# Kernel optimization log

Hardware: AMD Instinct MI355X
Metric: run time of the kernel (lower is better)

## Reference

```python
import jax, jax.numpy as jnp
import numpy as np

N_NODES = 50000
N_EDGES = 600000
DIM = 128
NUM_CLASSES = 10
EPS = 1e-15
MAX_NORM = 1.0 - 1e-5  # keep points strictly inside the unit ball for artanh


def _norm(x):
    return jnp.maximum(jnp.linalg.norm(x, axis=-1, keepdims=True), EPS)


def logmap0(x):
    # Poincare ball, c=1: artanh(||x||) * x / ||x||
    n = _norm(x)
    return jnp.arctanh(jnp.minimum(n, MAX_NORM)) * x / n


def expmap0(u):
    # Poincare ball, c=1: tanh(||u||) * u / ||u||
    n = _norm(u)
    return jnp.tanh(n) * u / n


def hyp_conv(x, W, b, src, dst):
    t = logmap0(x)                       # [N, D] manifold -> tangent at origin
    h = t @ W.T + b                      # [N, D] linear in tangent space
    y = expmap0(h)                       # [N, D] back to manifold
    # message passing: gather source features, scatter-add at destinations
    return jax.ops.segment_sum(y[src], dst, num_segments=N_NODES)


def setup_inputs() -> dict:
    key = jax.random.key(0)
    ks = jax.random.split(key, 8)
    edge_index = jax.random.randint(ks[0], (2, N_EDGES), 0, N_NODES, dtype=jnp.int64)
    # entity embeddings: small tangent vectors mapped onto the ball
    x = expmap0(0.01 * jax.random.normal(ks[1], (N_NODES, DIM), dtype=jnp.float32))
    s = 1.0 / np.sqrt(DIM)
    W1 = jax.random.normal(ks[2], (DIM, DIM), dtype=jnp.float32) * s
    b1 = jax.random.normal(ks[3], (DIM,), dtype=jnp.float32) * 0.01
    W2 = jax.random.normal(ks[4], (DIM, DIM), dtype=jnp.float32) * s
    b2 = jax.random.normal(ks[5], (DIM,), dtype=jnp.float32) * 0.01
    Wc = jax.random.normal(ks[6], (NUM_CLASSES, DIM), dtype=jnp.float32) * s
    bc = jax.random.normal(ks[7], (NUM_CLASSES,), dtype=jnp.float32) * 0.01
    return {"edge_index": edge_index, "x": x, "W1": W1, "b1": b1,
            "W2": W2, "b2": b2, "Wc": Wc, "bc": bc}


def reference(edge_index, x, W1, b1, W2, b2, Wc, bc):
    src, dst = edge_index[0], edge_index[1]
    h = hyp_conv(x, W1, b1, src, dst)
    h = jax.nn.relu(h)
    h = hyp_conv(h, W2, b2, src, dst)
    h = jax.nn.relu(h)
    t = logmap0(h)
    return t @ Wc.T + bc  # [N_NODES, NUM_CLASSES]
```

## Files before the change

### kernel.cpp

```cpp
#include <hip/hip_runtime.h>

#define N_NODES 50000
#define N_EDGES 600000
#define DIM 128
#define NCLS 10
#define ELLW 64
#define CURSTRIDE 16
#define EPSF 1e-15f
#define MAXNORM 0.99999f
#define NTILE ((N_NODES + 63) / 64)
#define FILLB 586
#define XFB 512

typedef __attribute__((ext_vector_type(8))) short bf16x8;
typedef __attribute__((ext_vector_type(4))) float f32x4;

__device__ inline float waveSum(float v) {
#pragma unroll
  for (int o = 1; o < 64; o <<= 1) v += __shfl_xor(v, o, 64);
  return v;
}

__device__ inline unsigned short f2bf(float f) {
  union { float f; unsigned u; } c; c.f = f;
  return (unsigned short)((c.u + 0x7FFFu + ((c.u >> 16) & 1u)) >> 16);
}
__device__ inline float bf_lo(unsigned u) {
  union { unsigned u; float f; } c; c.u = u << 16; return c.f;
}
__device__ inline float bf_hi(unsigned u) {
  union { unsigned u; float f; } c; c.u = u & 0xFFFF0000u; return c.f;
}

__global__ __launch_bounds__(256) void init_kernel(
    int* __restrict__ cursor, const float* __restrict__ W1, const float* __restrict__ W2,
    unsigned short* __restrict__ W1b, unsigned short* __restrict__ W2b)
{
  int i = blockIdx.x * 256 + threadIdx.x;
  if (i < N_NODES) cursor[i * CURSTRIDE] = 0;
  if (i < DIM * DIM) {
    W1b[i] = f2bf(W1[i]);
    W2b[i] = f2bf(W2[i]);
  }
}

__global__ __launch_bounds__(256, 2) void fill_transform(
    const int* __restrict__ src, const int* __restrict__ dst,
    int* __restrict__ cursor, unsigned short* __restrict__ ell,
    const float* __restrict__ x, const unsigned short* __restrict__ Wb,
    const float* __restrict__ b, unsigned short* __restrict__ y)
{
  __shared__ __align__(16) unsigned short At[64 * DIM];

  if (blockIdx.x < FILLB) {
    const int nthr = FILLB * 256;
    const int e = blockIdx.x * 256 + threadIdx.x;
    const int e0 = e, e1 = e + nthr, e2 = e + 2 * nthr, e3 = e + 3 * nthr;
    int d0, d1, d2, d3, s0, s1, s2, s3;
    if (e0 < N_EDGES) { d0 = dst[e0]; s0 = src[e0]; }
    if (e1 < N_EDGES) { d1 = dst[e1]; s1 = src[e1]; }
    if (e2 < N_EDGES) { d2 = dst[e2]; s2 = src[e2]; }
    if (e3 < N_EDGES) { d3 = dst[e3]; s3 = src[e3]; }
    int p0, p1, p2, p3;
    if (e0 < N_EDGES) p0 = atomicAdd(&cursor[d0 * CURSTRIDE], 1);
    if (e1 < N_EDGES) p1 = atomicAdd(&cursor[d1 * CURSTRIDE], 1);
    if (e2 < N_EDGES) p2 = atomicAdd(&cursor[d2 * CURSTRIDE], 1);
    if (e3 < N_EDGES) p3 = atomicAdd(&cursor[d3 * CURSTRIDE], 1);
    if (e0 < N_EDGES) ell[(size_t)d0 * ELLW + p0] = (unsigned short)s0;
    if (e1 < N_EDGES) ell[(size_t)d1 * ELLW + p1] = (unsigned short)s1;
    if (e2 < N_EDGES) ell[(size_t)d2 * ELLW + p2] = (unsigned short)s2;
    if (e3 < N_EDGES) ell[(size_t)d3 * ELLW + p3] = (unsigned short)s3;
    return;
  }

  const int tid = threadIdx.x;
  const int w = tid >> 6;
  const int l = tid & 63;
  const int lr = l & 15;
  const int lg = l >> 4;

  bf16x8 bf[8][4];
#pragma unroll
  for (int n = 0; n < 8; ++n)
#pragma unroll
    for (int kc = 0; kc < 4; ++kc)
      bf[n][kc] = *(const bf16x8*)(Wb + (n * 16 + lr) * DIM + kc * 32 + lg * 8);

  float bias[8];
#pragma unroll
  for (int n = 0; n < 8; ++n) bias[n] = b[n * 16 + lr];

  const int row = w * 16 + lr;

  for (int tile = blockIdx.x - FILLB; tile < NTILE; tile += XFB) {
    const int base = tile * 64;
    const int node = base + row;
    __syncthreads();

    float v[32];
    if (node < N_NODES) {
      const float4* xr = (const float4*)(x + (size_t)node * DIM + lg * 32);
#pragma unroll
      for (int q = 0; q < 8; ++q) {
        float4 f = xr[q];
        v[q * 4 + 0] = f.x; v[q * 4 + 1] = f.y; v[q * 4 + 2] = f.z; v[q * 4 + 3] = f.w;
      }
    } else {
#pragma unroll
      for (int q = 0; q < 32; ++q) v[q] = 0.f;
    }
    float sq = 0.f;
#pragma unroll
    for (int q = 0; q < 32; ++q) sq += v[q] * v[q];
    sq += __shfl_xor(sq, 16, 64);
    sq += __shfl_xor(sq, 32, 64);
    float n1 = sqrtf(sq);
    float nc = fmaxf(n1, EPSF);
    float nm = fminf(nc, MAXNORM);
    float scale = 0.5f * logf((1.f + nm) / (1.f - nm)) / nc;
#pragma unroll
    for (int s = 0; s < 4; ++s) {
      unsigned short tmp[8];
#pragma unroll
      for (int e = 0; e < 8; ++e) tmp[e] = f2bf(v[s * 8 + e] * scale);
      int byte = row * 256 + lg * 64 + s * 16;
      byte ^= (row & 7) << 4;
      *(bf16x8*)((char*)At + byte) = *(const bf16x8*)tmp;
    }
    __syncthreads();

    f32x4 acc[8];
#pragma unroll
    for (int n = 0; n < 8; ++n) {
      acc[n][0] = bias[n]; acc[n][1] = bias[n]; acc[n][2] = bias[n]; acc[n][3] = bias[n];
    }
#pragma unroll
    for (int kc = 0; kc < 4; ++kc) {
      int byte = row * 256 + kc * 64 + lg * 16;
      byte ^= (row & 7) << 4;
      bf16x8 af = *(const bf16x8*)((const char*)At + byte);
#pragma unroll
      for (int n = 0; n < 8; ++n)
        acc[n] = __builtin_amdgcn_mfma_f32_16x16x32_bf16(af, bf[n][kc], acc[n], 0, 0, 0);
    }

    float rs[4];
#pragma unroll
    for (int j = 0; j < 4; ++j) {
      float s2 = 0.f;
#pragma unroll
      for (int n = 0; n < 8; ++n) s2 += acc[n][j] * acc[n][j];
      s2 += __shfl_xor(s2, 1, 64);
      s2 += __shfl_xor(s2, 2, 64);
      s2 += __shfl_xor(s2, 4, 64);
      s2 += __shfl_xor(s2, 8, 64);
      float n2 = sqrtf(s2);
      float n2c = fmaxf(n2, EPSF);
      rs[j] = tanhf(n2c) / n2c;
    }
#pragma unroll
    for (int j = 0; j < 4; ++j) {
      int nrow = base + w * 16 + lg * 4 + j;
      if (nrow < N_NODES) {
        unsigned short* yr = y + (size_t)nrow * DIM + lr;
#pragma unroll
        for (int n = 0; n < 8; ++n) yr[n * 16] = f2bf(acc[n][j] * rs[j]);
      }
    }
  }
}

__global__ __launch_bounds__(256) void gatherT_kernel(
    const unsigned short* __restrict__ y, const int* __restrict__ cursor,
    const unsigned short* __restrict__ ell, unsigned short* __restrict__ tout)
{
  const int wave = threadIdx.x >> 6;
  const int lane = threadIdx.x & 63;
  const int nodeA = blockIdx.x * 8 + wave * 2;
  const int nodeB = nodeA + 1;

  const int cntA = cursor[nodeA * CURSTRIDE];
  const int cntB = cursor[nodeB * CURSTRIDE];
  const int idxA = (int)ell[(size_t)nodeA * ELLW + lane];
  const int idxB = (int)ell[(size_t)nodeB * ELLW + lane];

  float2 aA0 = {0.f, 0.f}, aA1 = {0.f, 0.f};
  float2 aB0 = {0.f, 0.f}, aB1 = {0.f, 0.f};

  unsigned uA[16], uB[16];
#pragma unroll
  for (int q = 0; q < 16; ++q) {
    int sA = __shfl(idxA, q, 64);
    int sB = __shfl(idxB, q, 64);
    uA[q] = ((const unsigned*)(y + (size_t)sA * DIM))[lane];
    uB[q] = ((const unsigned*)(y + (size_t)sB * DIM))[lane];
  }
#pragma unroll
  for (int q = 0; q < 16; ++q) {
    float vx = (q < cntA) ? bf_lo(uA[q]) : 0.f;
    float vy = (q < cntA) ? bf_hi(uA[q]) : 0.f;
    float wx = (q < cntB) ? bf_lo(uB[q]) : 0.f;
    float wy = (q < cntB) ? bf_hi(uB[q]) : 0.f;
    if (q & 1) { aA1.x += vx; aA1.y += vy; aB1.x += wx; aB1.y += wy; }
    else       { aA0.x += vx; aA0.y += vy; aB0.x += wx; aB0.y += wy; }
  }
  const int mx = max(cntA, cntB);
  for (int j = 16; j < mx; j += 8) {
    unsigned tA[8], tB[8];
#pragma unroll
    for (int q = 0; q < 8; ++q) {
      int sA = __shfl(idxA, j + q, 64);
      int sB = __shfl(idxB, j + q, 64);
      tA[q] = ((const unsigned*)(y + (size_t)sA * DIM))[lane];
      tB[q] = ((const unsigned*)(y + (size_t)sB * DIM))[lane];
    }
#pragma unroll
    for (int q = 0; q < 8; ++q) {
      if (j + q < cntA) { aA0.x += bf_lo(tA[q]); aA0.y += bf_hi(tA[q]); }
      if (j + q < cntB) { aB0.x += bf_lo(tB[q]); aB0.y += bf_hi(tB[q]); }
    }
  }

  float2 rA, rB;
  rA.x = fmaxf(aA0.x + aA1.x, 0.f);  rA.y = fmaxf(aA0.y + aA1.y, 0.f);
  rB.x = fmaxf(aB0.x + aB1.x, 0.f);  rB.y = fmaxf(aB0.y + aB1.y, 0.f);

  float sA = waveSum(rA.x * rA.x + rA.y * rA.y);
  float sB = waveSum(rB.x * rB.x + rB.y * rB.y);

  float nA = fmaxf(sqrtf(sA), EPSF);
  float nmA = fminf(nA, MAXNORM);
  float scA = 0.5f * logf((1.0f + nmA) / (1.0f - nmA)) / nA;
  float nB = fmaxf(sqrtf(sB), EPSF);
  float nmB = fminf(nB, MAXNORM);
  float scB = 0.5f * logf((1.0f + nmB) / (1.0f - nmB)) / nB;

  unsigned oA = (unsigned)f2bf(rA.x * scA) | ((unsigned)f2bf(rA.y * scA) << 16);
  unsigned oB = (unsigned)f2bf(rB.x * scB) | ((unsigned)f2bf(rB.y * scB) << 16);
  ((unsigned*)(tout + (size_t)nodeA * DIM))[lane] = oA;
  ((unsigned*)(tout + (size_t)nodeB * DIM))[lane] = oB;
}

__global__ __launch_bounds__(256, 2) void transform2_mfma(
    const unsigned short* __restrict__ t, const unsigned short* __restrict__ Wb,
    const float* __restrict__ b, unsigned short* __restrict__ y)
{
  const int tid = threadIdx.x;
  const int w = tid >> 6;
  const int l = tid & 63;
  const int lr = l & 15;
  const int lg = l >> 4;

  __shared__ __align__(16) unsigned short At[64 * DIM];

  bf16x8 bf[8][4];
#pragma unroll
  for (int n = 0; n < 8; ++n)
#pragma unroll
    for (int kc = 0; kc < 4; ++kc)
      bf[n][kc] = *(const bf16x8*)(Wb + (n * 16 + lr) * DIM + kc * 32 + lg * 8);

  float bias[8];
#pragma unroll
  for (int n = 0; n < 8; ++n) bias[n] = b[n * 16 + lr];

  const int row = w * 16 + lr;

  for (int tile = blockIdx.x; tile < NTILE; tile += gridDim.x) {
    const int base = tile * 64;
    const int node = base + row;
    __syncthreads();

#pragma unroll
    for (int s = 0; s < 4; ++s) {
      bf16x8 frag;
      if (node < N_NODES)
        frag = *(const bf16x8*)(t + (size_t)node * DIM + lg * 32 + s * 8);
      else
        frag = bf16x8{0, 0, 0, 0, 0, 0, 0, 0};
      int byte = row * 256 + lg * 64 + s * 16;
      byte ^= (row & 7) << 4;
      *(bf16x8*)((char*)At + byte) = frag;
    }
    __syncthreads();

    f32x4 acc[8];
#pragma unroll
    for (int n = 0; n < 8; ++n) {
      acc[n][0] = bias[n]; acc[n][1] = bias[n]; acc[n][2] = bias[n]; acc[n][3] = bias[n];
    }
#pragma unroll
    for (int kc = 0; kc < 4; ++kc) {
      int byte = row * 256 + kc * 64 + lg * 16;
      byte ^= (row & 7) << 4;
      bf16x8 af = *(const bf16x8*)((const char*)At + byte);
#pragma unroll
      for (int n = 0; n < 8; ++n)
        acc[n] = __builtin_amdgcn_mfma_f32_16x16x32_bf16(af, bf[n][kc], acc[n], 0, 0, 0);
    }

    float rs[4];
#pragma unroll
    for (int j = 0; j < 4; ++j) {
      float s2 = 0.f;
#pragma unroll
      for (int n = 0; n < 8; ++n) s2 += acc[n][j] * acc[n][j];
      s2 += __shfl_xor(s2, 1, 64);
      s2 += __shfl_xor(s2, 2, 64);
      s2 += __shfl_xor(s2, 4, 64);
      s2 += __shfl_xor(s2, 8, 64);
      float n2 = sqrtf(s2);
      float n2c = fmaxf(n2, EPSF);
      rs[j] = tanhf(n2c) / n2c;
    }
#pragma unroll
    for (int j = 0; j < 4; ++j) {
      int nrow = base + w * 16 + lg * 4 + j;
      if (nrow < N_NODES) {
        unsigned short* yr = y + (size_t)nrow * DIM + lr;
#pragma unroll
        for (int n = 0; n < 8; ++n) yr[n * 16] = f2bf(acc[n][j] * rs[j]);
      }
    }
  }
}

__global__ __launch_bounds__(256) void head_mfma(
    const unsigned short* __restrict__ t2, const float* __restrict__ Wc,
    const float* __restrict__ bc, float* __restrict__ out)
{
  const int base = blockIdx.x * 64;
  const int w = threadIdx.x >> 6;
  const int l = threadIdx.x & 63;
  const int lr = l & 15;
  const int lg = l >> 4;

  bf16x8 bw[4];
#pragma unroll
  for (int kc = 0; kc < 4; ++kc) {
    unsigned short tmp[8];
    if (lr < NCLS) {
      const float* wr = Wc + (size_t)lr * DIM + kc * 32 + lg * 8;
#pragma unroll
      for (int e = 0; e < 8; ++e) tmp[e] = f2bf(wr[e]);
    } else {
#pragma unroll
      for (int e = 0; e < 8; ++e) tmp[e] = 0;
    }
    bw[kc] = *(const bf16x8*)tmp;
  }
  const float bias = (lr < NCLS) ? bc[lr] : 0.f;

  const int arow = base + w * 16 + lr;
  f32x4 acc;
  acc[0] = bias; acc[1] = bias; acc[2] = bias; acc[3] = bias;
#pragma unroll
  for (int kc = 0; kc < 4; ++kc) {
    bf16x8 af;
    if (arow < N_NODES)
      af = *(const bf16x8*)(t2 + (size_t)arow * DIM + kc * 32 + lg * 8);
    else
      af = bf16x8{0, 0, 0, 0, 0, 0, 0, 0};
    acc = __builtin_amdgcn_mfma_f32_16x16x32_bf16(af, bw[kc], acc, 0, 0, 0);
  }

  if (lr < NCLS) {
#pragma unroll
    for (int j = 0; j < 4; ++j) {
      int nrow = base + w * 16 + lg * 4 + j;
      if (nrow < N_NODES) out[(size_t)nrow * NCLS + lr] = acc[j];
    }
  }
}

extern "C" void kernel_launch(void* const* d_in, const int* in_sizes, int n_in,
                              void* d_out, int out_size, void* d_ws, size_t ws_size,
                              hipStream_t stream)
{
  const int* edge = (const int*)d_in[0];
  const int* src = edge;
  const int* dst = edge + N_EDGES;
  const float* x  = (const float*)d_in[1];
  const float* W1 = (const float*)d_in[2];
  const float* b1 = (const float*)d_in[3];
  const float* W2 = (const float*)d_in[4];
  const float* b2 = (const float*)d_in[5];
  const float* Wc = (const float*)d_in[6];
  const float* bc = (const float*)d_in[7];
  float* out = (float*)d_out;

  unsigned short* ybuf = (unsigned short*)d_ws;
  unsigned short* tbuf = ybuf + (size_t)N_NODES * DIM;
  unsigned short* W1b = tbuf + (size_t)N_NODES * DIM;
  unsigned short* W2b = W1b + DIM * DIM;
  unsigned short* ell = W2b + DIM * DIM;
  int* cursor = (int*)(ell + (size_t)N_NODES * ELLW);

  init_kernel<<<(N_NODES + 255) / 256, 256, 0, stream>>>(cursor, W1, W2, W1b, W2b);

  fill_transform<<<FILLB + XFB, 256, 0, stream>>>(src, dst, cursor, ell, x, W1b, b1, ybuf);

  gatherT_kernel<<<N_NODES / 8, 256, 0, stream>>>(ybuf, cursor, ell, tbuf);

  transform2_mfma<<<512, 256, 0, stream>>>(tbuf, W2b, b2, ybuf);

  gatherT_kernel<<<N_NODES / 8, 256, 0, stream>>>(ybuf, cursor, ell, tbuf);

  head_mfma<<<NTILE, 256, 0, stream>>>(tbuf, Wc, bc, out);
}
```

Measured before the change: 127.2 us.

## Split node range to overlap gather of one half with dense transform of other

Each gather pass is split at a node boundary. The second half of the gather runs in the same launch as the dense transform (or the classifier head) of the first half, which the previous launch already gathered. A separate y2 buffer removes the in-place overwrite of ybuf so the two phases can coexist. This is meant to fill idle compute units and cut the tail of the memory-bound gather, at the cost of more launches and a mixed-role kernel that runs with the transform's launch bounds and shared memory.

```diff
diff --git a/kernel.cpp b/kernel.cpp
--- a/kernel.cpp
+++ b/kernel.cpp
@@ -8,9 +8,13 @@
 #define CURSTRIDE 16
 #define EPSF 1e-15f
 #define MAXNORM 0.99999f
-#define NTILE ((N_NODES + 63) / 64)
+#define NTILE 782
 #define FILLB 586
 #define XFB 512
+#define SPLIT 30784
+#define STILE 481
+#define GA_BLKS 3848
+#define GB_BLKS 2402
 
 typedef __attribute__((ext_vector_type(8))) short bf16x8;
 typedef __attribute__((ext_vector_type(4))) float f32x4;
@@ -170,13 +174,14 @@
   }
 }
 
-__global__ __launch_bounds__(256) void gatherT_kernel(
+__device__ __forceinline__ void do_gather2(
     const unsigned short* __restrict__ y, const int* __restrict__ cursor,
-    const unsigned short* __restrict__ ell, unsigned short* __restrict__ tout)
-{
-  const int wave = threadIdx.x >> 6;
+    const unsigned short* __restrict__ ell, unsigned short* __restrict__ tout,
+    int blkid, int nodeLo)
+{
+  const int wave = (int)threadIdx.x >> 6;
   const int lane = threadIdx.x & 63;
-  const int nodeA = blockIdx.x * 8 + wave * 2;
+  const int nodeA = nodeLo + blkid * 8 + wave * 2;
   const int nodeB = nodeA + 1;
 
   const int cntA = cursor[nodeA * CURSTRIDE];
@@ -241,17 +246,19 @@
   ((unsigned*)(tout + (size_t)nodeB * DIM))[lane] = oB;
 }
 
-__global__ __launch_bounds__(256, 2) void transform2_mfma(
+__device__ __forceinline__ void do_t2_tile(
     const unsigned short* __restrict__ t, const unsigned short* __restrict__ Wb,
-    const float* __restrict__ b, unsigned short* __restrict__ y)
+    const float* __restrict__ b, unsigned short* __restrict__ y,
+    unsigned short* At, int tile)
 {
   const int tid = threadIdx.x;
   const int w = tid >> 6;
   const int l = tid & 63;
   const int lr = l & 15;
   const int lg = l >> 4;
-
-  __shared__ __align__(16) unsigned short At[64 * DIM];
+  const int base = tile * 64;
+  const int row = w * 16 + lr;
+  const int node = base + row;
 
   bf16x8 bf[8][4];
 #pragma unroll
@@ -264,73 +271,65 @@
 #pragma unroll
   for (int n = 0; n < 8; ++n) bias[n] = b[n * 16 + lr];
 
-  const int row = w * 16 + lr;
-
-  for (int tile = blockIdx.x; tile < NTILE; tile += gridDim.x) {
-    const int base = tile * 64;
-    const int node = base + row;
-    __syncthreads();
-
-#pragma unroll
-    for (int s = 0; s < 4; ++s) {
-      bf16x8 frag;
-      if (node < N_NODES)
-        frag = *(const bf16x8*)(t + (size_t)node * DIM + lg * 32 + s * 8);
-      else
-        frag = bf16x8{0, 0, 0, 0, 0, 0, 0, 0};
-      int byte = row * 256 + lg * 64 + s * 16;
-      byte ^= (row & 7) << 4;
-      *(bf16x8*)((char*)At + byte) = frag;
-    }
-    __syncthreads();
-
-    f32x4 acc[8];
-#pragma unroll
-    for (int n = 0; n < 8; ++n) {
-      acc[n][0] = bias[n]; acc[n][1] = bias[n]; acc[n][2] = bias[n]; acc[n][3] = bias[n];
-    }
-#pragma unroll
-    for (int kc = 0; kc < 4; ++kc) {
-      int byte = row * 256 + kc * 64 + lg * 16;
-      byte ^= (row & 7) << 4;
-      bf16x8 af = *(const bf16x8*)((const char*)At + byte);
-#pragma unroll
-      for (int n = 0; n < 8; ++n)
-        acc[n] = __builtin_amdgcn_mfma_f32_16x16x32_bf16(af, bf[n][kc], acc[n], 0, 0, 0);
-    }
-
-    float rs[4];
-#pragma unroll
-    for (int j = 0; j < 4; ++j) {
-      float s2 = 0.f;
-#pragma unroll
-      for (int n = 0; n < 8; ++n) s2 += acc[n][j] * acc[n][j];
-      s2 += __shfl_xor(s2, 1, 64);
-      s2 += __shfl_xor(s2, 2, 64);
-      s2 += __shfl_xor(s2, 4, 64);
-      s2 += __shfl_xor(s2, 8, 64);
-      float n2 = sqrtf(s2);
-      float n2c = fmaxf(n2, EPSF);
-      rs[j] = tanhf(n2c) / n2c;
-    }
-#pragma unroll
-    for (int j = 0; j < 4; ++j) {
-      int nrow = base + w * 16 + lg * 4 + j;
-      if (nrow < N_NODES) {
-        unsigned short* yr = y + (size_t)nrow * DIM + lr;
-#pragma unroll
-        for (int n = 0; n < 8; ++n) yr[n * 16] = f2bf(acc[n][j] * rs[j]);
-      }
-    }
-  }
-}
-
-__global__ __launch_bounds__(256) void head_mfma(
+#pragma unroll
+  for (int s = 0; s < 4; ++s) {
+    bf16x8 frag;
+    if (node < N_NODES)
+      frag = *(const bf16x8*)(t + (size_t)node * DIM + lg * 32 + s * 8);
+    else
+      frag = bf16x8{0, 0, 0, 0, 0, 0, 0, 0};
+    int byte = row * 256 + lg * 64 + s * 16;
+    byte ^= (row & 7) << 4;
+    *(bf16x8*)((char*)At + byte) = frag;
+  }
+  __syncthreads();
+
+  f32x4 acc[8];
+#pragma unroll
+  for (int n = 0; n < 8; ++n) {
+    acc[n][0] = bias[n]; acc[n][1] = bias[n]; acc[n][2] = bias[n]; acc[n][3] = bias[n];
+  }
+#pragma unroll
+  for (int kc = 0; kc < 4; ++kc) {
+    int byte = row * 256 + kc * 64 + lg * 16;
+    byte ^= (row & 7) << 4;
+    bf16x8 af = *(const bf16x8*)((const char*)At + byte);
+#pragma unroll
+    for (int n = 0; n < 8; ++n)
+      acc[n] = __builtin_amdgcn_mfma_f32_16x16x32_bf16(af, bf[n][kc], acc[n], 0, 0, 0);
+  }
+
+  float rs[4];
+#pragma unroll
+  for (int j = 0; j < 4; ++j) {
+    float s2 = 0.f;
+#pragma unroll
+    for (int n = 0; n < 8; ++n) s2 += acc[n][j] * acc[n][j];
+    s2 += __shfl_xor(s2, 1, 64);
+    s2 += __shfl_xor(s2, 2, 64);
+    s2 += __shfl_xor(s2, 4, 64);
+    s2 += __shfl_xor(s2, 8, 64);
+    float n2 = sqrtf(s2);
+    float n2c = fmaxf(n2, EPSF);
+    rs[j] = tanhf(n2c) / n2c;
+  }
+#pragma unroll
+  for (int j = 0; j < 4; ++j) {
+    int nrow = base + w * 16 + lg * 4 + j;
+    if (nrow < N_NODES) {
+      unsigned short* yr = y + (size_t)nrow * DIM + lr;
+#pragma unroll
+      for (int n = 0; n < 8; ++n) yr[n * 16] = f2bf(acc[n][j] * rs[j]);
+    }
+  }
+}
+
+__device__ __forceinline__ void do_head_tile(
     const unsigned short* __restrict__ t2, const float* __restrict__ Wc,
-    const float* __restrict__ bc, float* __restrict__ out)
-{
-  const int base = blockIdx.x * 64;
-  const int w = threadIdx.x >> 6;
+    const float* __restrict__ bc, float* __restrict__ out, int tile)
+{
+  const int base = tile * 64;
+  const int w = (int)threadIdx.x >> 6;
   const int l = threadIdx.x & 63;
   const int lr = l & 15;
   const int lg = l >> 4;
@@ -371,6 +370,57 @@
       if (nrow < N_NODES) out[(size_t)nrow * NCLS + lr] = acc[j];
     }
   }
+}
+
+
+__global__ __launch_bounds__(256) void gather_range(
+    const unsigned short* __restrict__ y, const int* __restrict__ cursor,
+    const unsigned short* __restrict__ ell, unsigned short* __restrict__ tout,
+    int nodeLo)
+{
+  do_gather2(y, cursor, ell, tout, blockIdx.x, nodeLo);
+}
+
+__global__ __launch_bounds__(256, 2) void g1B_t2A(
+    const unsigned short* __restrict__ ybuf, const int* __restrict__ cursor,
+    const unsigned short* __restrict__ ell, unsigned short* __restrict__ tbuf,
+    const unsigned short* __restrict__ W2b, const float* __restrict__ b2,
+    unsigned short* __restrict__ y2buf)
+{
+  __shared__ __align__(16) unsigned short At[64 * DIM];
+  if (blockIdx.x < GB_BLKS) {
+    do_gather2(ybuf, cursor, ell, tbuf, blockIdx.x, SPLIT);
+  } else {
+    do_t2_tile(tbuf, W2b, b2, y2buf, At, blockIdx.x - GB_BLKS);
+  }
+}
+
+__global__ __launch_bounds__(256, 2) void t2B_kernel(
+    const unsigned short* __restrict__ tbuf, const unsigned short* __restrict__ W2b,
+    const float* __restrict__ b2, unsigned short* __restrict__ y2buf)
+{
+  __shared__ __align__(16) unsigned short At[64 * DIM];
+  do_t2_tile(tbuf, W2b, b2, y2buf, At, STILE + blockIdx.x);
+}
+
+__global__ __launch_bounds__(256) void g2B_headA(
+    const unsigned short* __restrict__ y2buf, const int* __restrict__ cursor,
+    const unsigned short* __restrict__ ell, unsigned short* __restrict__ tbuf,
+    const float* __restrict__ Wc, const float* __restrict__ bc,
+    float* __restrict__ out)
+{
+  if (blockIdx.x < GB_BLKS) {
+    do_gather2(y2buf, cursor, ell, tbuf, blockIdx.x, SPLIT);
+  } else {
+    do_head_tile(tbuf, Wc, bc, out, blockIdx.x - GB_BLKS);
+  }
+}
+
+__global__ __launch_bounds__(256) void headB_kernel(
+    const unsigned short* __restrict__ tbuf, const float* __restrict__ Wc,
+    const float* __restrict__ bc, float* __restrict__ out)
+{
+  do_head_tile(tbuf, Wc, bc, out, STILE + blockIdx.x);
 }
 
 extern "C" void kernel_launch(void* const* d_in, const int* in_sizes, int n_in,
@@ -389,9 +439,10 @@
   const float* bc = (const float*)d_in[7];
   float* out = (float*)d_out;
 
-  unsigned short* ybuf = (unsigned short*)d_ws;
-  unsigned short* tbuf = ybuf + (size_t)N_NODES * DIM;
-  unsigned short* W1b = tbuf + (size_t)N_NODES * DIM;
+  unsigned short* ybuf  = (unsigned short*)d_ws;
+  unsigned short* tbuf  = ybuf + (size_t)N_NODES * DIM;
+  unsigned short* y2buf = tbuf + (size_t)N_NODES * DIM;
+  unsigned short* W1b = y2buf + (size_t)N_NODES * DIM;
   unsigned short* W2b = W1b + DIM * DIM;
   unsigned short* ell = W2b + DIM * DIM;
   int* cursor = (int*)(ell + (size_t)N_NODES * ELLW);
@@ -400,11 +451,15 @@
 
   fill_transform<<<FILLB + XFB, 256, 0, stream>>>(src, dst, cursor, ell, x, W1b, b1, ybuf);
 
-  gatherT_kernel<<<N_NODES / 8, 256, 0, stream>>>(ybuf, cursor, ell, tbuf);
-
-  transform2_mfma<<<512, 256, 0, stream>>>(tbuf, W2b, b2, ybuf);
-
-  gatherT_kernel<<<N_NODES / 8, 256, 0, stream>>>(ybuf, cursor, ell, tbuf);
-
-  head_mfma<<<NTILE, 256, 0, stream>>>(tbuf, Wc, bc, out);
-}
+  gather_range<<<GA_BLKS, 256, 0, stream>>>(ybuf, cursor, ell, tbuf, 0);
+
+  g1B_t2A<<<GB_BLKS + STILE, 256, 0, stream>>>(ybuf, cursor, ell, tbuf, W2b, b2, y2buf);
+
+  t2B_kernel<<<NTILE - STILE, 256, 0, stream>>>(tbuf, W2b, b2, y2buf);
+
+  gather_range<<<GA_BLKS, 256, 0, stream>>>(y2buf, cursor, ell, tbuf, 0);
+
+  g2B_headA<<<GB_BLKS + STILE, 256, 0, stream>>>(y2buf, cursor, ell, tbuf, Wc, bc, out);
+
+  headB_kernel<<<NTILE - STILE, 256, 0, stream>>>(tbuf, Wc, bc, out);
+}
```

After: 141.7 us. 1.11x slower.
